# Kernel tuning notes

Hardware: AMD Instinct MI355X
Metric: run time of the kernel (lower is better)

## Reference

```python
import jax, jax.numpy as jnp
from jax import lax
import numpy as np

D_MODEL = 512
D_INNER = 1024      # expand=2
D_STATE = 256       # min(512, 256)
D_CONV = 4
DT_RANK = 32        # ceil(512/16)
N_FUSED = 64
EPS = 1e-5


def setup_inputs() -> dict:
    key = jax.random.key(0)
    ks = jax.random.split(key, 14)
    B, Lx = 4, 2048
    s = lambda k, shape: (jax.random.normal(k, shape, jnp.float32) * 0.02)
    return {
        "x": jax.random.normal(ks[0], (B, Lx, D_MODEL), jnp.float32),
        "fused_tokens": jax.random.normal(ks[1], (1, N_FUSED, D_MODEL), jnp.float32),
        "g1": jnp.ones((D_MODEL,), jnp.float32),
        "b1": jnp.zeros((D_MODEL,), jnp.float32),
        "g2": jnp.ones((D_MODEL,), jnp.float32),
        "b2": jnp.zeros((D_MODEL,), jnp.float32),
        "W_head": s(ks[2], (D_MODEL, D_MODEL)),
        "b_head": jnp.zeros((D_MODEL,), jnp.float32),
        "W_in": s(ks[3], (2 * D_INNER, D_MODEL)),          # in_proj, bias=False
        "W_conv": s(ks[4], (D_INNER, D_CONV)),             # depthwise causal conv
        "b_conv": s(ks[5], (D_INNER,)),
        "W_xp": s(ks[6], (DT_RANK + 2 * D_STATE, D_INNER)),  # x_proj, bias=False
        "W_dt": s(ks[7], (D_INNER, DT_RANK)),
        "b_dt": s(ks[8], (D_INNER,)),
        "A_log": jnp.log(jnp.broadcast_to(
            jnp.arange(1, D_STATE + 1, dtype=jnp.float32), (D_INNER, D_STATE))),
        "Dp": jnp.ones((D_INNER,), jnp.float32),           # skip parameter D
        "W_out": s(ks[9], (D_MODEL, D_INNER)),             # out_proj, bias=False
    }


def _ln(t, g, b):
    m = t.mean(-1, keepdims=True)
    v = t.var(-1, keepdims=True)
    return (t - m) * lax.rsqrt(v + EPS) * g + b


def _causal_dwconv(x, w, b):
    # x: (B, L, D); w: (D, K) depthwise kernel
    K = w.shape[1]
    xp = jnp.pad(x, ((0, 0), (K - 1, 0), (0, 0)))
    y = lax.conv_general_dilated(
        xp.transpose(0, 2, 1), w[:, None, :], (1,), 'VALID',
        feature_group_count=w.shape[0],
        dimension_numbers=('NCH', 'OIH', 'NCH'))
    return y.transpose(0, 2, 1) + b


def _selective_scan(u, delta, A, Bm, Cm, Dp):
    # u, delta: (B, L, Din); Bm, Cm: (B, L, N); A: (Din, N)
    B_, L, Din = u.shape
    N = A.shape[1]

    def step(h, inp):
        u_t, d_t, B_t, C_t = inp            # (B,Din),(B,Din),(B,N),(B,N)
        dA = jnp.exp(d_t[..., None] * A)    # (B, Din, N)
        h = dA * h + (d_t * u_t)[..., None] * B_t[:, None, :]
        y = jnp.einsum('bdn,bn->bd', h, C_t)
        return h, y

    h0 = jnp.zeros((B_, Din, N), u.dtype)
    xs = (u.transpose(1, 0, 2), delta.transpose(1, 0, 2),
          Bm.transpose(1, 0, 2), Cm.transpose(1, 0, 2))
    _, ys = lax.scan(step, h0, xs)
    return ys.transpose(1, 0, 2) + u * Dp


def reference(x, fused_tokens, g1, b1, g2, b2, W_head, b_head, W_in,
              W_conv, b_conv, W_xp, W_dt, b_dt, A_log, Dp, W_out):
    B = x.shape[0]
    toks = jnp.broadcast_to(fused_tokens, (B,) + fused_tokens.shape[1:])
    h = jnp.concatenate([x, toks], axis=1)          # (B, L, d)

    # --- Mamba block with pre-LN residual ---
    a = _ln(h, g1, b1)
    xz = a @ W_in.T                                 # (B, L, 2*Din)
    u, z = jnp.split(xz, 2, axis=-1)
    u = jax.nn.silu(_causal_dwconv(u, W_conv, b_conv))
    dbl = u @ W_xp.T                                # (B, L, dt_rank + 2N)
    dt, Bm, Cm = jnp.split(dbl, [DT_RANK, DT_RANK + D_STATE], axis=-1)
    delta = jax.nn.softplus(dt @ W_dt.T + b_dt)     # (B, L, Din)
    A = -jnp.exp(A_log)
    y = _selective_scan(u, delta, A, Bm, Cm, Dp)
    y = y * jax.nn.silu(z)
    h = y @ W_out.T + h

    # --- head with pre-LN residual ---
    h = _ln(h, g2, b2) @ W_head.T + b_head + h

    return h[:, -N_FUSED:, :]
```

## Files before the change

### kernel.cpp

```cpp
#include <hip/hip_runtime.h>

#define LTOT 2112
#define NROWS 8448
#define DM 512
#define DIN 1024
#define NST 256

using short8 = short  __attribute__((ext_vector_type(8)));
using f32x4  = float  __attribute__((ext_vector_type(4)));

__device__ __forceinline__ float fast_silu(float x){ return x / (1.f + __expf(-x)); }

__device__ __forceinline__ unsigned short f2bf(float f){
  unsigned u = __float_as_uint(f);
  unsigned r = (u + 0x7FFFu + ((u >> 16) & 1u)) >> 16;
  return (unsigned short)r;
}

__global__ __launch_bounds__(256) void ln1_kernel(
    const float* __restrict__ x, const float* __restrict__ toks,
    const float* __restrict__ g1, const float* __restrict__ b1,
    float* __restrict__ a, unsigned short* __restrict__ abf,
    unsigned short* __restrict__ a_last)
{
  int r = blockIdx.x;
  int bb = r / LTOT, t = r - bb*LTOT;
  const float* row = (t < 2048) ? (x + ((size_t)bb*2048 + t)*DM)
                                : (toks + (size_t)(t - 2048)*DM);
  int tid = threadIdx.x;
  float v0 = row[tid], v1 = row[tid + 256];
  float s = v0 + v1, sq = v0*v0 + v1*v1;
  #pragma unroll
  for (int o = 32; o > 0; o >>= 1){ s += __shfl_down(s,o); sq += __shfl_down(sq,o); }
  __shared__ float sb[8];
  if ((tid & 63) == 0){ sb[tid>>6] = s; sb[4 + (tid>>6)] = sq; }
  __syncthreads();
  float S  = sb[0]+sb[1]+sb[2]+sb[3];
  float SQ = sb[4]+sb[5]+sb[6]+sb[7];
  float mean = S * (1.f/DM);
  float var  = SQ * (1.f/DM) - mean*mean;
  float rs = rsqrtf(var + 1e-5f);
  size_t o0 = (size_t)r*DM;
  float r0 = (v0 - mean)*rs*g1[tid]       + b1[tid];
  float r1 = (v1 - mean)*rs*g1[tid + 256] + b1[tid + 256];
  a[o0 + tid]       = r0;
  a[o0 + tid + 256] = r1;
  unsigned short h0 = f2bf(r0), h1 = f2bf(r1);
  abf[o0 + tid]       = h0;
  abf[o0 + tid + 256] = h1;
  if (t >= 2048) {
    size_t lr = (size_t)(bb*64 + (t - 2048))*DM;
    a_last[lr + tid]       = h0;
    a_last[lr + tid + 256] = h1;
  }
}

__global__ __launch_bounds__(256) void f32_to_bf16_kernel(
    const float* __restrict__ in, unsigned short* __restrict__ out, int n4)
{
  int i = blockIdx.x*256 + threadIdx.x;
  if (i >= n4) return;
  float4 v = reinterpret_cast<const float4*>(in)[i];
  ushort4 o;
  o.x = f2bf(v.x); o.y = f2bf(v.y); o.z = f2bf(v.z); o.w = f2bf(v.w);
  reinterpret_cast<ushort4*>(out)[i] = o;
}

__global__ __launch_bounds__(256) void gemm_bf16(
    const unsigned short* __restrict__ A, const unsigned short* __restrict__ W,
    float* __restrict__ C, int M, int N, int K, int ldc)
{
  __shared__ unsigned short As[128][40];
  __shared__ unsigned short Bs[64][40];
  int tid  = threadIdx.x;
  int lane = tid & 63, wid = tid >> 6;
  int wm = wid >> 1, wn = wid & 1;
  int l15 = lane & 15, l4 = lane >> 4;
  int m0 = blockIdx.x * 128, n0 = blockIdx.y * 64;
  int sr = tid >> 2, sc = (tid & 3) * 8;

  f32x4 acc[4][2];
  #pragma unroll
  for (int i = 0; i < 4; ++i)
    #pragma unroll
    for (int j = 0; j < 2; ++j) acc[i][j] = (f32x4)0.f;

  for (int k0 = 0; k0 < K; k0 += 32) {
    #pragma unroll
    for (int rr = 0; rr < 2; ++rr) {
      int r = sr + rr*64;
      uint4 v = *reinterpret_cast<const uint4*>(A + (size_t)(m0 + r)*K + k0 + sc);
      *reinterpret_cast<uint4*>(&As[r][sc]) = v;
    }
    {
      int col = n0 + sr;
      uint4 v = make_uint4(0u,0u,0u,0u);
      if (col < N) v = *reinterpret_cast<const uint4*>(W + (size_t)col*K + k0 + sc);
      *reinterpret_cast<uint4*>(&Bs[sr][sc]) = v;
    }
    __syncthreads();
    short8 bfrag[2];
    #pragma unroll
    for (int fn = 0; fn < 2; ++fn)
      bfrag[fn] = *reinterpret_cast<const short8*>(&Bs[wn*32 + fn*16 + l15][l4*8]);
    #pragma unroll
    for (int fm = 0; fm < 4; ++fm) {
      short8 afrag = *reinterpret_cast<const short8*>(&As[wm*64 + fm*16 + l15][l4*8]);
      acc[fm][0] = __builtin_amdgcn_mfma_f32_16x16x32_bf16(afrag, bfrag[0], acc[fm][0], 0, 0, 0);
      acc[fm][1] = __builtin_amdgcn_mfma_f32_16x16x32_bf16(afrag, bfrag[1], acc[fm][1], 0, 0, 0);
    }
    __syncthreads();
  }
  #pragma unroll
  for (int fm = 0; fm < 4; ++fm)
    #pragma unroll
    for (int fn = 0; fn < 2; ++fn) {
      int col = n0 + wn*32 + fn*16 + l15;
      if (col < N)
        #pragma unroll
        for (int j = 0; j < 4; ++j) {
          int row = m0 + wm*64 + fm*16 + l4*4 + j;
          C[(size_t)row*ldc + col] = acc[fm][fn][j];
        }
    }
}

__global__ __launch_bounds__(256) void conv_silu_kernel(
    const float* __restrict__ upre, const float* __restrict__ Wc,
    const float* __restrict__ bc, float* __restrict__ u,
    unsigned short* __restrict__ ubf, unsigned short* __restrict__ u_last)
{
  size_t idx = (size_t)blockIdx.x*256 + threadIdx.x;
  int d = (int)(idx & 1023);
  int r = (int)(idx >> 10);
  int t = r % LTOT;
  float4 w4 = *reinterpret_cast<const float4*>(Wc + (size_t)d*4);
  float acc = bc[d];
  const float* up = upre + idx;
  if (t >= 3) acc = fmaf(up[-3*DIN], w4.x, acc);
  if (t >= 2) acc = fmaf(up[-2*DIN], w4.y, acc);
  if (t >= 1) acc = fmaf(up[-1*DIN], w4.z, acc);
  acc = fmaf(up[0], w4.w, acc);
  float res = fast_silu(acc);
  u[idx] = res;
  unsigned short hb = f2bf(res);
  ubf[idx] = hb;
  if (t >= 2048) {
    int bb = r / LTOT;
    u_last[(size_t)(bb*64 + (t - 2048))*DIN + d] = hb;
  }
}

__global__ __launch_bounds__(256) void delta_kernel(
    const float* __restrict__ dbl, const float* __restrict__ W_dt,
    const float* __restrict__ b_dt, const float* __restrict__ u,
    float* __restrict__ deltaT, float* __restrict__ duT)
{
  __shared__ float dts[32][33];
  __shared__ float wds[32][33];
  __shared__ float dT[32][33];
  __shared__ float uT[32][33];
  int r0 = blockIdx.x * 32;
  int d0 = blockIdx.y * 32;
  int bb = r0 / LTOT, t0 = r0 % LTOT;
  int tid = threadIdx.x;
  #pragma unroll
  for (int p = 0; p < 4; ++p) {
    int o = tid + p*256;
    int rl = o >> 5, j = o & 31;
    dts[rl][j] = dbl[(size_t)(r0 + rl)*288 + j];
    wds[rl][j] = W_dt[(size_t)(d0 + rl)*32 + j];
  }
  __syncthreads();
  #pragma unroll
  for (int p = 0; p < 4; ++p) {
    int o = tid + p*256;
    int dl = o & 31, rl = o >> 5;
    float acc = b_dt[d0 + dl];
    #pragma unroll
    for (int j = 0; j < 32; ++j) acc = fmaf(dts[rl][j], wds[dl][j], acc);
    float delta = (acc > 20.f) ? acc : __logf(1.f + __expf(acc));
    float uu = u[(size_t)(r0 + rl)*DIN + d0 + dl];
    dT[dl][rl] = delta;
    uT[dl][rl] = delta * uu;
  }
  __syncthreads();
  #pragma unroll
  for (int p = 0; p < 4; ++p) {
    int o = tid + p*256;
    int dl = o >> 5, ti = o & 31;
    size_t gi = ((size_t)bb*DIN + d0 + dl)*LTOT + t0 + ti;
    deltaT[gi] = dT[dl][ti];
    duT[gi]    = uT[dl][ti];
  }
}

__global__ __launch_bounds__(256) void scan_kernel(
    const float* __restrict__ deltaT, const float* __restrict__ duT,
    const float* __restrict__ dbl, const float* __restrict__ Cm,
    const float* __restrict__ A_log, float* __restrict__ y)
{
  int blk = blockIdx.x;
  int bb = blk >> 9;
  int d0 = (blk & 511) << 1;
  int n = threadIdx.x;
  float Ak[2], h[2] = {0.f, 0.f};
  #pragma unroll
  for (int g = 0; g < 2; ++g) {
    float al = A_log[(size_t)(d0+g)*NST + n];
    Ak[g] = -__builtin_amdgcn_exp2f(al * 1.44269504089f) * 1.44269504089f;
  }
  const size_t basebd = ((size_t)bb*DIN + d0)*LTOT;
  const float* __restrict__ pd = deltaT + basebd;
  const float* __restrict__ pu = duT    + basebd;
  const float* __restrict__ Bp = dbl + (size_t)bb*LTOT*288 + 32 + n;

  for (int t0c = 0; t0c < 2048; t0c += 4) {
    float Bnv[4];
    #pragma unroll
    for (int i = 0; i < 4; ++i) Bnv[i] = Bp[(size_t)(t0c + i)*288];
    float dv[2][4], uv[2][4];
    #pragma unroll
    for (int g = 0; g < 2; ++g) {
      float4 dq = *reinterpret_cast<const float4*>(pd + (size_t)g*LTOT + t0c);
      float4 uq = *reinterpret_cast<const float4*>(pu + (size_t)g*LTOT + t0c);
      dv[g][0]=dq.x; dv[g][1]=dq.y; dv[g][2]=dq.z; dv[g][3]=dq.w;
      uv[g][0]=uq.x; uv[g][1]=uq.y; uv[g][2]=uq.z; uv[g][3]=uq.w;
    }
    #pragma unroll
    for (int i = 0; i < 4; ++i) {
      float Bn = Bnv[i];
      #pragma unroll
      for (int g = 0; g < 2; ++g) {
        float dA = __builtin_amdgcn_exp2f(dv[g][i] * Ak[g]);
        h[g] = fmaf(dA, h[g], uv[g][i] * Bn);
      }
    }
  }

  __shared__ float red[4][2];
  for (int t = 2048; t < 2112; ++t) {
    float Bn = Bp[(size_t)t*288];
    #pragma unroll
    for (int g = 0; g < 2; ++g) {
      float dA = __builtin_amdgcn_exp2f(pd[(size_t)g*LTOT + t] * Ak[g]);
      h[g] = fmaf(dA, h[g], pu[(size_t)g*LTOT + t] * Bn);
    }
    float Cn = Cm[((size_t)(bb*64 + (t - 2048)))*NST + n];
    #pragma unroll
    for (int g = 0; g < 2; ++g) {
      float v = h[g] * Cn;
      #pragma unroll
      for (int o = 32; o > 0; o >>= 1) v += __shfl_down(v, o);
      if ((threadIdx.x & 63) == 0) red[threadIdx.x >> 6][g] = v;
    }
    __syncthreads();
    if (threadIdx.x < 2) {
      float sv = red[0][threadIdx.x] + red[1][threadIdx.x]
               + red[2][threadIdx.x] + red[3][threadIdx.x];
      y[((size_t)(bb*64 + (t - 2048)))*DIN + d0 + threadIdx.x] = sv;
    }
    __syncthreads();
  }
}

__global__ __launch_bounds__(256) void y2_kernel(
    const float* __restrict__ y, const float* __restrict__ u, const float* __restrict__ zs,
    const float* __restrict__ Dp, float* __restrict__ y2)
{
  int idx = blockIdx.x*256 + threadIdx.x;
  int rr = idx >> 10, d = idx & 1023;
  int bb = rr >> 6, tt = rr & 63;
  size_t r = (size_t)bb*LTOT + 2048 + tt;
  float yv = y[idx] + u[r*DIN + d] * Dp[d];
  y2[idx] = yv * fast_silu(zs[idx]);
}

__global__ __launch_bounds__(256) void outproj_kernel(
    const float* __restrict__ y2, const float* __restrict__ Wout,
    const float* __restrict__ toks, float* __restrict__ hfin)
{
  __shared__ float ys[4][DIN];
  int rb = blockIdx.x;
  int tid = threadIdx.x;
  #pragma unroll
  for (int rr = 0; rr < 4; ++rr)
    #pragma unroll
    for (int j = 0; j < 4; ++j)
      ys[rr][tid + j*256] = y2[(size_t)(rb*4 + rr)*DIN + tid + j*256];
  __syncthreads();
  #pragma unroll
  for (int cj = 0; cj < 2; ++cj) {
    int cidx = tid + cj*256;
    const float* wr = Wout + (size_t)cidx*DIN;
    float a0=0.f,a1=0.f,a2=0.f,a3=0.f;
    for (int k = 0; k < DIN; k += 4) {
      float4 w4 = *reinterpret_cast<const float4*>(wr + k);
      float4 r0 = *reinterpret_cast<const float4*>(&ys[0][k]);
      float4 r1 = *reinterpret_cast<const float4*>(&ys[1][k]);
      float4 r2 = *reinterpret_cast<const float4*>(&ys[2][k]);
      float4 r3 = *reinterpret_cast<const float4*>(&ys[3][k]);
      a0=fmaf(r0.x,w4.x,a0); a0=fmaf(r0.y,w4.y,a0); a0=fmaf(r0.z,w4.z,a0); a0=fmaf(r0.w,w4.w,a0);
      a1=fmaf(r1.x,w4.x,a1); a1=fmaf(r1.y,w4.y,a1); a1=fmaf(r1.z,w4.z,a1); a1=fmaf(r1.w,w4.w,a1);
      a2=fmaf(r2.x,w4.x,a2); a2=fmaf(r2.y,w4.y,a2); a2=fmaf(r2.z,w4.z,a2); a2=fmaf(r2.w,w4.w,a2);
      a3=fmaf(r3.x,w4.x,a3); a3=fmaf(r3.y,w4.y,a3); a3=fmaf(r3.z,w4.z,a3); a3=fmaf(r3.w,w4.w,a3);
    }
    float accs[4] = {a0,a1,a2,a3};
    #pragma unroll
    for (int rr = 0; rr < 4; ++rr) {
      int rg = rb*4 + rr;
      hfin[(size_t)rg*DM + cidx] = accs[rr] + toks[(size_t)(rg & 63)*DM + cidx];
    }
  }
}

__global__ __launch_bounds__(256) void head_kernel(
    const float* __restrict__ hfin, const float* __restrict__ g2, const float* __restrict__ b2,
    const float* __restrict__ Wh, const float* __restrict__ bh, float* __restrict__ out)
{
  int rr = blockIdx.x;
  int tid = threadIdx.x;
  float v0 = hfin[(size_t)rr*DM + tid];
  float v1 = hfin[(size_t)rr*DM + tid + 256];
  float s = v0 + v1, sq = v0*v0 + v1*v1;
  #pragma unroll
  for (int o = 32; o > 0; o >>= 1){ s += __shfl_down(s,o); sq += __shfl_down(sq,o); }
  __shared__ float sb[8];
  if ((tid & 63) == 0){ sb[tid>>6] = s; sb[4 + (tid>>6)] = sq; }
  __syncthreads();
  float S  = sb[0]+sb[1]+sb[2]+sb[3];
  float SQ = sb[4]+sb[5]+sb[6]+sb[7];
  float mean = S * (1.f/DM);
  float rs = rsqrtf(SQ * (1.f/DM) - mean*mean + 1e-5f);
  __shared__ float as[DM];
  as[tid]       = (v0 - mean)*rs*g2[tid]       + b2[tid];
  as[tid + 256] = (v1 - mean)*rs*g2[tid + 256] + b2[tid + 256];
  __syncthreads();
  #pragma unroll
  for (int cj = 0; cj < 2; ++cj) {
    int cidx = tid + cj*256;
    const float* wr = Wh + (size_t)cidx*DM;
    float acc = bh[cidx] + (cj ? v1 : v0);
    for (int k = 0; k < DM; k += 4) {
      float4 w4 = *reinterpret_cast<const float4*>(wr + k);
      float4 a4 = *reinterpret_cast<const float4*>(&as[k]);
      acc = fmaf(a4.x,w4.x,acc); acc = fmaf(a4.y,w4.y,acc);
      acc = fmaf(a4.z,w4.z,acc); acc = fmaf(a4.w,w4.w,acc);
    }
    out[(size_t)rr*DM + cidx] = acc;
  }
}

extern "C" void kernel_launch(void* const* d_in, const int* in_sizes, int n_in,
                              void* d_out, int out_size, void* d_ws, size_t ws_size,
                              hipStream_t stream) {
  const float* x      = (const float*)d_in[0];
  const float* toks   = (const float*)d_in[1];
  const float* g1     = (const float*)d_in[2];
  const float* b1     = (const float*)d_in[3];
  const float* g2     = (const float*)d_in[4];
  const float* b2     = (const float*)d_in[5];
  const float* W_head = (const float*)d_in[6];
  const float* b_head = (const float*)d_in[7];
  const float* W_in   = (const float*)d_in[8];
  const float* W_conv = (const float*)d_in[9];
  const float* b_conv = (const float*)d_in[10];
  const float* W_xp   = (const float*)d_in[11];
  const float* W_dt   = (const float*)d_in[12];
  const float* b_dt   = (const float*)d_in[13];
  const float* A_log  = (const float*)d_in[14];
  const float* Dp     = (const float*)d_in[15];
  const float* W_out  = (const float*)d_in[16];

  float* ws = (float*)d_ws;
  float* a_buf   = ws;
  float* u_pre   = a_buf   + (size_t)NROWS*DM;
  float* u_buf   = u_pre   + (size_t)NROWS*DIN;
  float* dbl_buf = u_buf   + (size_t)NROWS*DIN;
  float* duT     = dbl_buf + (size_t)NROWS*288;
  float* zs      = duT     + (size_t)NROWS*DIN;
  float* Cm      = zs      + (size_t)256*DIN;
  float* y_buf   = Cm      + (size_t)256*NST;
  float* y2_buf  = y_buf   + (size_t)256*DIN;
  float* hfin    = y2_buf  + (size_t)256*DIN;
  float* tail    = hfin    + (size_t)256*DM;
  float* deltaT  = u_pre;

  unsigned short* a_last_bf16 = (unsigned short*)tail;
  unsigned short* u_last_bf16 = a_last_bf16 + (size_t)256*DM;

  unsigned short* a_bf16  = (unsigned short*)duT;
  unsigned short* u_bf16  = a_bf16 + (size_t)NROWS*DM;
  unsigned short* wi_bf16 = u_bf16 + (size_t)NROWS*DIN;
  unsigned short* wx_bf16 = wi_bf16 + (size_t)2*DIN*DM;

  f32_to_bf16_kernel<<<(2*DIN*DM/4 + 255)/256, 256, 0, stream>>>(W_in, wi_bf16, 2*DIN*DM/4);
  f32_to_bf16_kernel<<<(544*DIN/4 + 255)/256, 256, 0, stream>>>(W_xp, wx_bf16, 544*DIN/4);

  ln1_kernel<<<NROWS, 256, 0, stream>>>(x, toks, g1, b1, a_buf, a_bf16, a_last_bf16);
  gemm_bf16<<<dim3(NROWS/128, DIN/64), 256, 0, stream>>>(a_bf16, wi_bf16, u_pre,
                                                         NROWS, DIN, DM, DIN);
  gemm_bf16<<<dim3(2, DIN/64), 256, 0, stream>>>(a_last_bf16, wi_bf16 + (size_t)DIN*DM,
                                                 zs, 256, DIN, DM, DIN);
  conv_silu_kernel<<<(NROWS*DIN)/256, 256, 0, stream>>>(u_pre, W_conv, b_conv,
                                                        u_buf, u_bf16, u_last_bf16);
  gemm_bf16<<<dim3(NROWS/128, (288 + 63)/64), 256, 0, stream>>>(u_bf16, wx_bf16, dbl_buf,
                                                                NROWS, 288, DIN, 288);
  gemm_bf16<<<dim3(2, NST/64), 256, 0, stream>>>(u_last_bf16, wx_bf16 + (size_t)288*DIN,
                                                 Cm, 256, NST, DIN, NST);
  delta_kernel<<<dim3(NROWS/32, DIN/32), 256, 0, stream>>>(dbl_buf, W_dt, b_dt, u_buf,
                                                           deltaT, duT);
  scan_kernel<<<2048, 256, 0, stream>>>(deltaT, duT, dbl_buf, Cm, A_log, y_buf);
  y2_kernel<<<1024, 256, 0, stream>>>(y_buf, u_buf, zs, Dp, y2_buf);
  outproj_kernel<<<64, 256, 0, stream>>>(y2_buf, W_out, toks, hfin);
  head_kernel<<<256, 256, 0, stream>>>(hfin, g2, b2, W_head, b_head, (float*)d_out);
}
```

Baseline: 709.1 us.

## Fuse small kernels, drop dead LN fp32 output, deepen scan unroll

Several independent tweaks. The unused fp32 LayerNorm output store is removed, and the two weight-conversion launches are merged into one kernel. The y2 gating kernel is folded into the out-projection load. The scan loop now processes 8 timesteps per iteration and gains a launch-bounds occupancy hint. Together these aim to cut launch overhead and memory traffic, with possible register-pressure changes in the scan.

```diff
diff --git a/kernel.cpp b/kernel.cpp
--- a/kernel.cpp
+++ b/kernel.cpp
@@ -20,8 +20,7 @@
 __global__ __launch_bounds__(256) void ln1_kernel(
     const float* __restrict__ x, const float* __restrict__ toks,
     const float* __restrict__ g1, const float* __restrict__ b1,
-    float* __restrict__ a, unsigned short* __restrict__ abf,
-    unsigned short* __restrict__ a_last)
+    unsigned short* __restrict__ abf, unsigned short* __restrict__ a_last)
 {
   int r = blockIdx.x;
   int bb = r / LTOT, t = r - bb*LTOT;
@@ -43,8 +42,6 @@
   size_t o0 = (size_t)r*DM;
   float r0 = (v0 - mean)*rs*g1[tid]       + b1[tid];
   float r1 = (v1 - mean)*rs*g1[tid + 256] + b1[tid + 256];
-  a[o0 + tid]       = r0;
-  a[o0 + tid + 256] = r1;
   unsigned short h0 = f2bf(r0), h1 = f2bf(r1);
   abf[o0 + tid]       = h0;
   abf[o0 + tid + 256] = h1;
@@ -55,12 +52,16 @@
   }
 }
 
-__global__ __launch_bounds__(256) void f32_to_bf16_kernel(
-    const float* __restrict__ in, unsigned short* __restrict__ out, int n4)
-{
+__global__ __launch_bounds__(256) void w2bf_kernel(
+    const float* __restrict__ Wi, const float* __restrict__ Wx,
+    unsigned short* __restrict__ out)
+{
+  const int NWI4  = (2*DIN*DM)/4;
+  const int NTOT4 = NWI4 + (544*DIN)/4;
   int i = blockIdx.x*256 + threadIdx.x;
-  if (i >= n4) return;
-  float4 v = reinterpret_cast<const float4*>(in)[i];
+  if (i >= NTOT4) return;
+  const float* src = (i < NWI4) ? (Wi + (size_t)i*4) : (Wx + (size_t)(i - NWI4)*4);
+  float4 v = *reinterpret_cast<const float4*>(src);
   ushort4 o;
   o.x = f2bf(v.x); o.y = f2bf(v.y); o.z = f2bf(v.z); o.w = f2bf(v.w);
   reinterpret_cast<ushort4*>(out)[i] = o;
@@ -195,7 +196,7 @@
   }
 }
 
-__global__ __launch_bounds__(256) void scan_kernel(
+__global__ __launch_bounds__(256, 8) void scan_kernel(
     const float* __restrict__ deltaT, const float* __restrict__ duT,
     const float* __restrict__ dbl, const float* __restrict__ Cm,
     const float* __restrict__ A_log, float* __restrict__ y)
@@ -215,20 +216,24 @@
   const float* __restrict__ pu = duT    + basebd;
   const float* __restrict__ Bp = dbl + (size_t)bb*LTOT*288 + 32 + n;
 
-  for (int t0c = 0; t0c < 2048; t0c += 4) {
-    float Bnv[4];
-    #pragma unroll
-    for (int i = 0; i < 4; ++i) Bnv[i] = Bp[(size_t)(t0c + i)*288];
-    float dv[2][4], uv[2][4];
+  for (int t0c = 0; t0c < 2048; t0c += 8) {
+    float Bnv[8];
+    #pragma unroll
+    for (int i = 0; i < 8; ++i) Bnv[i] = Bp[(size_t)(t0c + i)*288];
+    float dv[2][8], uv[2][8];
     #pragma unroll
     for (int g = 0; g < 2; ++g) {
-      float4 dq = *reinterpret_cast<const float4*>(pd + (size_t)g*LTOT + t0c);
-      float4 uq = *reinterpret_cast<const float4*>(pu + (size_t)g*LTOT + t0c);
-      dv[g][0]=dq.x; dv[g][1]=dq.y; dv[g][2]=dq.z; dv[g][3]=dq.w;
-      uv[g][0]=uq.x; uv[g][1]=uq.y; uv[g][2]=uq.z; uv[g][3]=uq.w;
-    }
-    #pragma unroll
-    for (int i = 0; i < 4; ++i) {
+      float4 dq0 = *reinterpret_cast<const float4*>(pd + (size_t)g*LTOT + t0c);
+      float4 dq1 = *reinterpret_cast<const float4*>(pd + (size_t)g*LTOT + t0c + 4);
+      float4 uq0 = *reinterpret_cast<const float4*>(pu + (size_t)g*LTOT + t0c);
+      float4 uq1 = *reinterpret_cast<const float4*>(pu + (size_t)g*LTOT + t0c + 4);
+      dv[g][0]=dq0.x; dv[g][1]=dq0.y; dv[g][2]=dq0.z; dv[g][3]=dq0.w;
+      dv[g][4]=dq1.x; dv[g][5]=dq1.y; dv[g][6]=dq1.z; dv[g][7]=dq1.w;
+      uv[g][0]=uq0.x; uv[g][1]=uq0.y; uv[g][2]=uq0.z; uv[g][3]=uq0.w;
+      uv[g][4]=uq1.x; uv[g][5]=uq1.y; uv[g][6]=uq1.z; uv[g][7]=uq1.w;
+    }
+    #pragma unroll
+    for (int i = 0; i < 8; ++i) {
       float Bn = Bnv[i];
       #pragma unroll
       for (int g = 0; g < 2; ++g) {
@@ -264,30 +269,28 @@
   }
 }
 
-__global__ __launch_bounds__(256) void y2_kernel(
-    const float* __restrict__ y, const float* __restrict__ u, const float* __restrict__ zs,
-    const float* __restrict__ Dp, float* __restrict__ y2)
-{
-  int idx = blockIdx.x*256 + threadIdx.x;
-  int rr = idx >> 10, d = idx & 1023;
-  int bb = rr >> 6, tt = rr & 63;
-  size_t r = (size_t)bb*LTOT + 2048 + tt;
-  float yv = y[idx] + u[r*DIN + d] * Dp[d];
-  y2[idx] = yv * fast_silu(zs[idx]);
-}
-
 __global__ __launch_bounds__(256) void outproj_kernel(
-    const float* __restrict__ y2, const float* __restrict__ Wout,
-    const float* __restrict__ toks, float* __restrict__ hfin)
+    const float* __restrict__ y, const float* __restrict__ u,
+    const float* __restrict__ zs, const float* __restrict__ Dp,
+    const float* __restrict__ Wout, const float* __restrict__ toks,
+    float* __restrict__ hfin)
 {
   __shared__ float ys[4][DIN];
   int rb = blockIdx.x;
   int tid = threadIdx.x;
   #pragma unroll
-  for (int rr = 0; rr < 4; ++rr)
-    #pragma unroll
-    for (int j = 0; j < 4; ++j)
-      ys[rr][tid + j*256] = y2[(size_t)(rb*4 + rr)*DIN + tid + j*256];
+  for (int rr = 0; rr < 4; ++rr) {
+    int rg = rb*4 + rr;
+    int bbb = rg >> 6, tt = rg & 63;
+    size_t rfull = (size_t)bbb*LTOT + 2048 + tt;
+    #pragma unroll
+    for (int j = 0; j < 4; ++j) {
+      int d = tid + j*256;
+      size_t idx = (size_t)rg*DIN + d;
+      float yv = y[idx] + u[rfull*DIN + d] * Dp[d];
+      ys[rr][d] = yv * fast_silu(zs[idx]);
+    }
+  }
   __syncthreads();
   #pragma unroll
   for (int cj = 0; cj < 2; ++cj) {
@@ -394,10 +397,12 @@
   unsigned short* wi_bf16 = u_bf16 + (size_t)NROWS*DIN;
   unsigned short* wx_bf16 = wi_bf16 + (size_t)2*DIN*DM;
 
-  f32_to_bf16_kernel<<<(2*DIN*DM/4 + 255)/256, 256, 0, stream>>>(W_in, wi_bf16, 2*DIN*DM/4);
-  f32_to_bf16_kernel<<<(544*DIN/4 + 255)/256, 256, 0, stream>>>(W_xp, wx_bf16, 544*DIN/4);
-
-  ln1_kernel<<<NROWS, 256, 0, stream>>>(x, toks, g1, b1, a_buf, a_bf16, a_last_bf16);
+  {
+    const int NTOT4 = (2*DIN*DM + 544*DIN)/4;
+    w2bf_kernel<<<(NTOT4 + 255)/256, 256, 0, stream>>>(W_in, W_xp, wi_bf16);
+  }
+
+  ln1_kernel<<<NROWS, 256, 0, stream>>>(x, toks, g1, b1, a_bf16, a_last_bf16);
   gemm_bf16<<<dim3(NROWS/128, DIN/64), 256, 0, stream>>>(a_bf16, wi_bf16, u_pre,
                                                          NROWS, DIN, DM, DIN);
   gemm_bf16<<<dim3(2, DIN/64), 256, 0, stream>>>(a_last_bf16, wi_bf16 + (size_t)DIN*DM,
@@ -411,7 +416,6 @@
   delta_kernel<<<dim3(NROWS/32, DIN/32), 256, 0, stream>>>(dbl_buf, W_dt, b_dt, u_buf,
                                                            deltaT, duT);
   scan_kernel<<<2048, 256, 0, stream>>>(deltaT, duT, dbl_buf, Cm, A_log, y_buf);
-  y2_kernel<<<1024, 256, 0, stream>>>(y_buf, u_buf, zs, Dp, y2_buf);
-  outproj_kernel<<<64, 256, 0, stream>>>(y2_buf, W_out, toks, hfin);
+  outproj_kernel<<<64, 256, 0, stream>>>(y_buf, u_buf, zs, Dp, W_out, toks, hfin);
   head_kernel<<<256, 256, 0, stream>>>(hfin, g2, b2, W_head, b_head, (float*)d_out);
 }
```

New measurement: 712.2 us. About the same (+0.4%).
